# Optimization experiments

Hardware: AMD Instinct MI355X
Metric: run time of the kernel (lower is better)

The kernel has to match this reference:

```python
import jax, jax.numpy as jnp
import numpy as np

N_NODES = 100000
N_EDGES = 3200000
N_FEAT = 256
HIDDEN = 64
N_CLASSES = 6


def gcn_conv(x, W, b, src, dst, n_nodes):
    """PyG GCNConv: out = D^{-1/2} (A + I) D^{-1/2} X W + b (self-loops added)."""
    h = x @ W  # [N, out]
    loops = jnp.arange(n_nodes, dtype=src.dtype)
    src2 = jnp.concatenate([src, loops])
    dst2 = jnp.concatenate([dst, loops])
    # degree over destination nodes (edge weight 1), including self-loops
    deg = jax.ops.segment_sum(jnp.ones_like(dst2, dtype=h.dtype), dst2,
                              num_segments=n_nodes)
    dis = jnp.where(deg > 0, jax.lax.rsqrt(deg), 0.0)  # deg^{-1/2}
    norm = dis[src2] * dis[dst2]  # [E+N]
    msg = h[src2] * norm[:, None]  # gather + scale
    out = jax.ops.segment_sum(msg, dst2, num_segments=n_nodes)  # scatter-add
    return out + b


def setup_inputs() -> dict:
    key = jax.random.key(0)
    ks = jax.random.split(key, 5)
    x = jax.random.normal(ks[0], (N_NODES, N_FEAT), dtype=jnp.float32)
    edge_index = jax.random.randint(ks[1], (2, N_EDGES), 0, N_NODES, dtype=jnp.int64)
    W1 = jax.random.normal(ks[2], (N_FEAT, HIDDEN), dtype=jnp.float32) / np.sqrt(N_FEAT)
    b1 = jnp.zeros((HIDDEN,), dtype=jnp.float32)
    W2 = jax.random.normal(ks[3], (HIDDEN, HIDDEN), dtype=jnp.float32) / np.sqrt(HIDDEN)
    b2 = jnp.zeros((HIDDEN,), dtype=jnp.float32)
    Wfc = jax.random.normal(ks[4], (HIDDEN, N_CLASSES), dtype=jnp.float32) / np.sqrt(HIDDEN)
    bfc = jnp.zeros((N_CLASSES,), dtype=jnp.float32)
    return {"x": x, "edge_index": edge_index, "W1": W1, "b1": b1,
            "W2": W2, "b2": b2, "Wfc": Wfc, "bfc": bfc}


def reference(x, edge_index, W1, b1, W2, b2, Wfc, bfc):
    src, dst = edge_index[0], edge_index[1]
    n = x.shape[0]
    h = jax.nn.relu(gcn_conv(x, W1, b1, src, dst, n))
    # dropout(p=0.2) is identity in eval mode
    h = jax.nn.relu(gcn_conv(h, W2, b2, src, dst, n))
    return h @ Wfc + bfc
```

## Files before the change

kernel.cpp:

```cpp
#include <hip/hip_runtime.h>
#include <hip/hip_fp16.h>
#include <math.h>

#define NFEAT 256
#define HID 64
#define NCLS 6
#define CAP 4096
#define NBMX 1600
#define RCAP 8
#define CHUNK 16384
#define ROUND 1024
#define FUSED_LDS 57856

typedef float vf4 __attribute__((ext_vector_type(4)));
typedef int   vi4 __attribute__((ext_vector_type(4)));


__global__ __launch_bounds__(256) void k_zero_int(int* __restrict__ p, int n) {
  int i = blockIdx.x * 256 + threadIdx.x;
  if (i < n) p[i] = 0;
}


__global__ __launch_bounds__(256) void k_fused(const int* __restrict__ src,
                                               const int* __restrict__ dst,
                                               int* __restrict__ gcur,
                                               unsigned* __restrict__ packed,
                                               int E, int nbuck, int nbb,
                                               const float* __restrict__ X,
                                               const float* __restrict__ W1,
                                               __half* __restrict__ H16, int n) {
  extern __shared__ char smem[];
  int t = threadIdx.x;

  if (blockIdx.x < nbb) {
    unsigned* ring = (unsigned*)smem;
    int* basel = (int*)(smem + NBMX * RCAP * 4);
    for (int i = t; i < nbuck; i += 256) basel[i] = 0;
    __syncthreads();

    int e0 = blockIdx.x * CHUNK;
    int e1 = e0 + CHUNK;
    if (e1 > E) e1 = E;

    for (int r0 = e0; r0 < e1; r0 += ROUND) {
      int i0 = r0 + t * 4;
      int s4[4], d4[4];
      bool full = (i0 + 4 <= e1);
      if (full) {
        vi4 sv = __builtin_nontemporal_load((const vi4*)&src[i0]);
        vi4 dv = __builtin_nontemporal_load((const vi4*)&dst[i0]);
        s4[0] = sv.x; s4[1] = sv.y; s4[2] = sv.z; s4[3] = sv.w;
        d4[0] = dv.x; d4[1] = dv.y; d4[2] = dv.z; d4[3] = dv.w;
      } else {
        for (int q = 0; q < 4; ++q)
          if (i0 + q < e1) { s4[q] = src[i0 + q]; d4[q] = dst[i0 + q]; }
      }
#pragma unroll
      for (int q = 0; q < 4; ++q) {
        if (i0 + q < e1) {
          int b = d4[q] >> 6;
          unsigned e = ((unsigned)s4[q] << 6) | (unsigned)(d4[q] & 63);
          int sl = atomicAdd(&basel[b], 1);
          if (sl < RCAP) ring[b * RCAP + sl] = e;
          else packed[(size_t)b * CAP + atomicAdd(&gcur[b], 1)] = e;
        }
      }
      __syncthreads();
      for (int b = t; b < nbuck; b += 256) {
        if (basel[b] >= RCAP) {
          int gb = atomicAdd(&gcur[b], RCAP);
          unsigned* pd = &packed[(size_t)b * CAP + gb];
#pragma unroll
          for (int k = 0; k < RCAP; ++k) pd[k] = ring[b * RCAP + k];
          basel[b] = 0;
        }
      }
      __syncthreads();
    }
    for (int b = t; b < nbuck; b += 256) {
      int m = basel[b];
      if (m > 0) {
        int gb = atomicAdd(&gcur[b], m);
        unsigned* pd = &packed[(size_t)b * CAP + gb];
        for (int k = 0; k < m; ++k) pd[k] = ring[b * RCAP + k];
      }
    }
  } else {
    float* Wl = (float*)smem;
    float* Xl = Wl + 4096;
    const int row0 = (blockIdx.x - nbb) * 64;
    const int tc = t & 15;
    const int tr = t >> 4;
    float acc[4][4] = {};

    for (int k0 = 0; k0 < NFEAT; k0 += 64) {
      __syncthreads();
#pragma unroll
      for (int i = 0; i < 4; ++i) {
        int idx = t * 4 + i * 1024;
        int kr = idx >> 6, c = idx & 63;
        *(vf4*)&Wl[idx] = *(const vf4*)&W1[(size_t)(k0 + kr) * 64 + c];
      }
#pragma unroll
      for (int i = 0; i < 4; ++i) {
        int idx = t * 4 + i * 1024;
        int r = idx >> 6, c = idx & 63;
        int row = row0 + r;
        vf4 v = {0.f, 0.f, 0.f, 0.f};
        if (row < n) v = __builtin_nontemporal_load((const vf4*)&X[(size_t)row * NFEAT + k0 + c]);
        *(vf4*)&Xl[idx] = v;
      }
      __syncthreads();
#pragma unroll 4
      for (int kk = 0; kk < 64; kk += 4) {
        float4 xv[4], wv[4];
#pragma unroll
        for (int r = 0; r < 4; ++r) xv[r] = *(float4*)&Xl[(tr * 4 + r) * 64 + kk];
#pragma unroll
        for (int q = 0; q < 4; ++q) wv[q] = *(float4*)&Wl[(kk + q) * 64 + tc * 4];
#pragma unroll
        for (int r = 0; r < 4; ++r) {
          const float xr[4] = {xv[r].x, xv[r].y, xv[r].z, xv[r].w};
#pragma unroll
          for (int q = 0; q < 4; ++q) {
            acc[r][0] += xr[q] * wv[q].x;
            acc[r][1] += xr[q] * wv[q].y;
            acc[r][2] += xr[q] * wv[q].z;
            acc[r][3] += xr[q] * wv[q].w;
          }
        }
      }
    }
#pragma unroll
    for (int r = 0; r < 4; ++r) {
      int row = row0 + tr * 4 + r;
      if (row < n) {
        __half2 h01 = __floats2half2_rn(acc[r][0], acc[r][1]);
        __half2 h23 = __floats2half2_rn(acc[r][2], acc[r][3]);
        uint2 st;
        st.x = *reinterpret_cast<unsigned*>(&h01);
        st.y = *reinterpret_cast<unsigned*>(&h23);
        ((uint2*)H16)[(size_t)row * 16 + tc] = st;
      }
    }
  }
}


__global__ __launch_bounds__(256) void k_build(unsigned* __restrict__ packed,
                                               const int* __restrict__ gcur,
                                               int2* __restrict__ rowrange,
                                               float* __restrict__ dis,
                                               int n, int nbuck) {
  __shared__ unsigned buf[CAP];
  __shared__ unsigned outb[CAP];
  __shared__ int cnt4[4][64];
  __shared__ int cur4[4][64];
  __shared__ int offi[64];
  __shared__ int offx[64];
  __shared__ int cntl[64];
  int b = blockIdx.x;
  int t = threadIdx.x;
  int g = t >> 6;
  int m = gcur[b];
  if (m > CAP) m = CAP;
  unsigned* pb = packed + (size_t)b * CAP;

  cnt4[g][t & 63] = 0;
  for (int k = t; k < m; k += 256) buf[k] = pb[k];
  __syncthreads();
  for (int k = t; k < m; k += 256) atomicAdd(&cnt4[g][buf[k] & 63u], 1);
  __syncthreads();
  if (t < 64) {
    int c0 = cnt4[0][t], c1 = cnt4[1][t], c2 = cnt4[2][t], c3 = cnt4[3][t];
    int tot = c0 + c1 + c2 + c3;
    cntl[t] = tot;
    offi[t] = tot;
    cur4[0][t] = 0;
    cur4[1][t] = c0;
    cur4[2][t] = c0 + c1;
    cur4[3][t] = c0 + c1 + c2;
  }
  __syncthreads();
  for (int off = 1; off < 64; off <<= 1) {
    int x = (t < 64) ? offi[t] : 0;
    int y = (t >= off && t < 64) ? offi[t - off] : 0;
    __syncthreads();
    if (t < 64) offi[t] = x + y;
    __syncthreads();
  }
  if (t < 64) {
    offx[t] = offi[t] - cntl[t];
    int v = b * 64 + t;
    if (v < n) {
      rowrange[v] = make_int2(b * CAP + offx[t], cntl[t]);
      dis[v] = rsqrtf((float)cntl[t] + 1.0f);
    }
#pragma unroll
    for (int gg = 0; gg < 4; ++gg) cur4[gg][t] += offx[t];
  }
  __syncthreads();
  for (int k = t; k < m; k += 256) {
    unsigned e = buf[k];
    int dl = e & 63u;
    int q = atomicAdd(&cur4[g][dl], 1);
    outb[q] = e >> 6;
  }
  __syncthreads();
  for (int k = t; k < m; k += 256) pb[k] = outb[k];
}


__global__ __launch_bounds__(256) void k_agg_w(const int2* __restrict__ rowrange,
                                               const int* __restrict__ srcs,
                                               const __half* __restrict__ g16,
                                               const float* __restrict__ dis,
                                               const float* __restrict__ bias,
                                               float* __restrict__ outp, int n) {
  int v = blockIdx.x * 16 + (threadIdx.x >> 4);
  if (v >= n) return;
  int lane = threadIdx.x & 15;
  int2 rr = rowrange[v];
  int j = rr.x, end = rr.x + rr.y;
  const uint2* g2 = (const uint2*)g16;

  float dv = dis[v];
  uint2 su = g2[(size_t)v * 16 + lane];
  float2 f0 = __half22float2(*reinterpret_cast<__half2*>(&su.x));
  float2 f1 = __half22float2(*reinterpret_cast<__half2*>(&su.y));
  float ax = dv * f0.x, ay = dv * f0.y, az = dv * f1.x, aw = dv * f1.y;

  for (; j + 8 <= end; j += 8) {
    int s[8];
#pragma unroll
    for (int q = 0; q < 8; ++q) s[q] = __builtin_nontemporal_load(&srcs[j + q]);
    float ds[8];
    uint2 a[8];
#pragma unroll
    for (int q = 0; q < 8; ++q) { ds[q] = dis[s[q]]; a[q] = g2[(size_t)s[q] * 16 + lane]; }
#pragma unroll
    for (int q = 0; q < 8; ++q) {
      float2 p0 = __half22float2(*reinterpret_cast<__half2*>(&a[q].x));
      float2 p1 = __half22float2(*reinterpret_cast<__half2*>(&a[q].y));
      ax = fmaf(ds[q], p0.x, ax); ay = fmaf(ds[q], p0.y, ay);
      az = fmaf(ds[q], p1.x, az); aw = fmaf(ds[q], p1.y, aw);
    }
  }
  for (; j < end; ++j) {
    int s0 = __builtin_nontemporal_load(&srcs[j]);
    float ds = dis[s0];
    uint2 a0 = g2[(size_t)s0 * 16 + lane];
    float2 p0 = __half22float2(*reinterpret_cast<__half2*>(&a0.x));
    float2 p1 = __half22float2(*reinterpret_cast<__half2*>(&a0.y));
    ax = fmaf(ds, p0.x, ax); ay = fmaf(ds, p0.y, ay);
    az = fmaf(ds, p1.x, az); aw = fmaf(ds, p1.y, aw);
  }

  float4 bb = *(const float4*)&bias[lane * 4];
  float4 o;
  o.x = fmaxf(fmaf(dv, ax, bb.x), 0.f);
  o.y = fmaxf(fmaf(dv, ay, bb.y), 0.f);
  o.z = fmaxf(fmaf(dv, az, bb.z), 0.f);
  o.w = fmaxf(fmaf(dv, aw, bb.w), 0.f);
  ((float4*)outp)[(size_t)v * 16 + lane] = o;
}


template<int K>
__global__ __launch_bounds__(256) void k_gemm_scaled(const float* __restrict__ X,
                                                     const float* __restrict__ W,
                                                     const float* __restrict__ dis,
                                                     __half* __restrict__ G16, int n) {
  __shared__ float Wl[64 * 64];
  __shared__ float Xl[64 * 64];
  const int tid = threadIdx.x;
  const int row0 = blockIdx.x * 64;
  const int tc = tid & 15;
  const int tr = tid >> 4;
  float acc[4][4] = {};

  for (int k0 = 0; k0 < K; k0 += 64) {
    __syncthreads();
#pragma unroll
    for (int i = 0; i < 4; ++i) {
      int idx = tid * 4 + i * 1024;
      int kr = idx >> 6, c = idx & 63;
      *(vf4*)&Wl[idx] = *(const vf4*)&W[(size_t)(k0 + kr) * 64 + c];
    }
#pragma unroll
    for (int i = 0; i < 4; ++i) {
      int idx = tid * 4 + i * 1024;
      int r = idx >> 6, c = idx & 63;
      int row = row0 + r;
      vf4 v = {0.f, 0.f, 0.f, 0.f};
      if (row < n) v = __builtin_nontemporal_load((const vf4*)&X[(size_t)row * K + k0 + c]);
      *(vf4*)&Xl[idx] = v;
    }
    __syncthreads();
#pragma unroll 4
    for (int kk = 0; kk < 64; kk += 4) {
      float4 xv[4], wv[4];
#pragma unroll
      for (int r = 0; r < 4; ++r) xv[r] = *(float4*)&Xl[(tr * 4 + r) * 64 + kk];
#pragma unroll
      for (int q = 0; q < 4; ++q) wv[q] = *(float4*)&Wl[(kk + q) * 64 + tc * 4];
#pragma unroll
      for (int r = 0; r < 4; ++r) {
        const float xr[4] = {xv[r].x, xv[r].y, xv[r].z, xv[r].w};
#pragma unroll
        for (int q = 0; q < 4; ++q) {
          acc[r][0] += xr[q] * wv[q].x;
          acc[r][1] += xr[q] * wv[q].y;
          acc[r][2] += xr[q] * wv[q].z;
          acc[r][3] += xr[q] * wv[q].w;
        }
      }
    }
  }
#pragma unroll
  for (int r = 0; r < 4; ++r) {
    int row = row0 + tr * 4 + r;
    if (row < n) {
      float s = dis[row];
      __half2 h01 = __floats2half2_rn(acc[r][0] * s, acc[r][1] * s);
      __half2 h23 = __floats2half2_rn(acc[r][2] * s, acc[r][3] * s);
      uint2 st;
      st.x = *reinterpret_cast<unsigned*>(&h01);
      st.y = *reinterpret_cast<unsigned*>(&h23);
      ((uint2*)G16)[(size_t)row * 16 + tc] = st;
    }
  }
}


__global__ __launch_bounds__(256) void k_agg_csr(const int2* __restrict__ rowrange,
                                                 const int* __restrict__ srcs,
                                                 const __half* __restrict__ g16,
                                                 const float* __restrict__ dis,
                                                 const float* __restrict__ bias,
                                                 float* __restrict__ outp, int n) {
  int v = blockIdx.x * 16 + (threadIdx.x >> 4);
  if (v >= n) return;
  int lane = threadIdx.x & 15;
  int2 rr = rowrange[v];
  int j = rr.x, end = rr.x + rr.y;
  const uint2* g2 = (const uint2*)g16;

  uint2 su = g2[(size_t)v * 16 + lane];
  float2 f0 = __half22float2(*reinterpret_cast<__half2*>(&su.x));
  float2 f1 = __half22float2(*reinterpret_cast<__half2*>(&su.y));
  float ax = f0.x, ay = f0.y, az = f1.x, aw = f1.y;

  for (; j + 8 <= end; j += 8) {
    int s[8];
#pragma unroll
    for (int q = 0; q < 8; ++q) s[q] = __builtin_nontemporal_load(&srcs[j + q]);
    uint2 a[8];
#pragma unroll
    for (int q = 0; q < 8; ++q) a[q] = g2[(size_t)s[q] * 16 + lane];
#pragma unroll
    for (int q = 0; q < 8; ++q) {
      float2 p0 = __half22float2(*reinterpret_cast<__half2*>(&a[q].x));
      float2 p1 = __half22float2(*reinterpret_cast<__half2*>(&a[q].y));
      ax += p0.x; ay += p0.y; az += p1.x; aw += p1.y;
    }
  }
  for (; j < end; ++j) {
    int s0 = __builtin_nontemporal_load(&srcs[j]);
    uint2 a0 = g2[(size_t)s0 * 16 + lane];
    float2 p0 = __half22float2(*reinterpret_cast<__half2*>(&a0.x));
    float2 p1 = __half22float2(*reinterpret_cast<__half2*>(&a0.y));
    ax += p0.x; ay += p0.y; az += p1.x; aw += p1.y;
  }

  float dv = dis[v];
  float4 bb = *(const float4*)&bias[lane * 4];
  float4 o;
  o.x = fmaxf(fmaf(dv, ax, bb.x), 0.f);
  o.y = fmaxf(fmaf(dv, ay, bb.y), 0.f);
  o.z = fmaxf(fmaf(dv, az, bb.z), 0.f);
  o.w = fmaxf(fmaf(dv, aw, bb.w), 0.f);
  ((float4*)outp)[(size_t)v * 16 + lane] = o;
}


__global__ __launch_bounds__(256) void k_fc(const float* __restrict__ A,
                                            const float* __restrict__ Wfc,
                                            const float* __restrict__ bfc,
                                            float* __restrict__ outp, int n) {
  __shared__ float Wl[64 * NCLS];
  __shared__ float bl[8];
  int tid = threadIdx.x;
  for (int i = tid; i < 64 * NCLS; i += 256) Wl[i] = Wfc[i];
  if (tid < NCLS) bl[tid] = bfc[tid];
  __syncthreads();
  int row = blockIdx.x * 256 + tid;
  if (row >= n) return;
  float accv[NCLS];
#pragma unroll
  for (int j = 0; j < NCLS; ++j) accv[j] = bl[j];
  const vf4* a4 = (const vf4*)&A[(size_t)row * 64];
#pragma unroll
  for (int k4 = 0; k4 < 16; ++k4) {
    vf4 a = __builtin_nontemporal_load(&a4[k4]);
    const float av[4] = {a.x, a.y, a.z, a.w};
#pragma unroll
    for (int q = 0; q < 4; ++q)
#pragma unroll
      for (int j = 0; j < NCLS; ++j) accv[j] += av[q] * Wl[(k4 * 4 + q) * NCLS + j];
  }
#pragma unroll
  for (int j = 0; j < NCLS; ++j) outp[(size_t)row * NCLS + j] = accv[j];
}


extern "C" void kernel_launch(void* const* d_in, const int* in_sizes, int n_in,
                              void* d_out, int out_size, void* d_ws, size_t ws_size,
                              hipStream_t stream) {
  const float* x   = (const float*)d_in[0];
  const int*   ei  = (const int*)d_in[1];
  const float* W1  = (const float*)d_in[2];
  const float* b1  = (const float*)d_in[3];
  const float* W2  = (const float*)d_in[4];
  const float* b2  = (const float*)d_in[5];
  const float* Wfc = (const float*)d_in[6];
  const float* bfc = (const float*)d_in[7];
  float* out = (float*)d_out;

  const int n = in_sizes[0] / NFEAT;
  const int E = in_sizes[1] / 2;
  const int* src = ei;
  const int* dst = ei + E;
  const int nbuck = (n + 63) >> 6;
  const int nbb = (E + CHUNK - 1) / CHUNK;
  const int ntile = (n + 63) / 64;

  char* ws = (char*)d_ws;
  size_t off = 0;
  auto alloc = [&](size_t bytes) -> void* {
    void* p = (void*)(ws + off);
    off += (bytes + 255) & ~(size_t)255;
    return p;
  };
  float* dis      = (float*)alloc((size_t)n * 4);
  int2*  rowrange = (int2*)alloc((size_t)n * 8);
  int*   gcur     = (int*)alloc((size_t)nbuck * 4);
  unsigned* packed = (unsigned*)alloc((size_t)nbuck * CAP * 4);
  __half* bufA16  = (__half*)alloc((size_t)n * HID * 2);
  float* bufB     = (float*)alloc((size_t)n * HID * 4);

  k_zero_int<<<(nbuck + 255) / 256, 256, 0, stream>>>(gcur, nbuck);
  k_fused<<<nbb + ntile, 256, FUSED_LDS, stream>>>(src, dst, gcur, packed, E, nbuck, nbb,
                                                   x, W1, bufA16, n);
  k_build<<<nbuck, 256, 0, stream>>>(packed, gcur, rowrange, dis, n, nbuck);

  k_agg_w<<<(n + 15) / 16, 256, 0, stream>>>(rowrange, (const int*)packed, bufA16, dis, b1, bufB, n);

  k_gemm_scaled<HID><<<(n + 63) / 64, 256, 0, stream>>>(bufB, W2, dis, bufA16, n);
  k_agg_csr<<<(n + 15) / 16, 256, 0, stream>>>(rowrange, (const int*)packed, bufA16, dis, b2, bufB, n);

  k_fc<<<(n + 255) / 256, 256, 0, stream>>>(bufB, Wfc, bfc, out, n);
}
```

Before: 319.8 us.

## Replace atomic bucket rings with count-scan-scatter edge bucketing

Replaces the LDS ring-buffer plus global-atomic bucketing of edges with a two-pass scheme. A count kernel builds per-block bucket histograms, a single-block scan turns them into exact offsets, and the fused kernel then scatters edges directly to precomputed slots in a compact E-sized array. This removes the global atomics and per-round syncs, and drops the fixed per-bucket capacity padding. The cost is an extra read of dst, two added launches, and a serial single-block scan over about 196x1563 counts.

```diff
diff --git a/kernel.cpp b/kernel.cpp
--- a/kernel.cpp
+++ b/kernel.cpp
@@ -5,26 +5,95 @@
 #define NFEAT 256
 #define HID 64
 #define NCLS 6
-#define CAP 4096
 #define NBMX 1600
-#define RCAP 8
+#define CAPB 4096
 #define CHUNK 16384
-#define ROUND 1024
-#define FUSED_LDS 57856
+#define FUSED_LDS 32768
 
 typedef float vf4 __attribute__((ext_vector_type(4)));
 typedef int   vi4 __attribute__((ext_vector_type(4)));
 
 
-__global__ __launch_bounds__(256) void k_zero_int(int* __restrict__ p, int n) {
-  int i = blockIdx.x * 256 + threadIdx.x;
-  if (i < n) p[i] = 0;
+__global__ __launch_bounds__(256) void k_count(const int* __restrict__ dst,
+                                               int* __restrict__ C, int E, int nbuck) {
+  __shared__ int cnt[NBMX];
+  int t = threadIdx.x;
+  for (int i = t; i < nbuck; i += 256) cnt[i] = 0;
+  __syncthreads();
+  int e0 = blockIdx.x * CHUNK;
+  int e1 = e0 + CHUNK;
+  if (e1 > E) e1 = E;
+  for (int r0 = e0; r0 < e1; r0 += 1024) {
+    int i0 = r0 + t * 4;
+    if (i0 + 4 <= e1) {
+      vi4 dv = __builtin_nontemporal_load((const vi4*)&dst[i0]);
+      atomicAdd(&cnt[dv.x >> 6], 1);
+      atomicAdd(&cnt[dv.y >> 6], 1);
+      atomicAdd(&cnt[dv.z >> 6], 1);
+      atomicAdd(&cnt[dv.w >> 6], 1);
+    } else {
+      for (int q = 0; q < 4; ++q)
+        if (i0 + q < e1) atomicAdd(&cnt[dst[i0 + q] >> 6], 1);
+    }
+  }
+  __syncthreads();
+  int* Crow = C + (size_t)blockIdx.x * nbuck;
+  for (int i = t; i < nbuck; i += 256) Crow[i] = cnt[i];
+}
+
+
+__global__ __launch_bounds__(256) void k_scan(int* __restrict__ C,
+                                              int* __restrict__ T,
+                                              int* __restrict__ bbase,
+                                              int nblk, int nbuck) {
+  __shared__ int sh[256];
+  __shared__ int carry;
+  int t = threadIdx.x;
+  for (int b = t; b < nbuck; b += 256) {
+    int run = 0;
+    int blk = 0;
+    for (; blk + 4 <= nblk; blk += 4) {
+      int c0 = C[(size_t)(blk + 0) * nbuck + b];
+      int c1 = C[(size_t)(blk + 1) * nbuck + b];
+      int c2 = C[(size_t)(blk + 2) * nbuck + b];
+      int c3 = C[(size_t)(blk + 3) * nbuck + b];
+      C[(size_t)(blk + 0) * nbuck + b] = run; run += c0;
+      C[(size_t)(blk + 1) * nbuck + b] = run; run += c1;
+      C[(size_t)(blk + 2) * nbuck + b] = run; run += c2;
+      C[(size_t)(blk + 3) * nbuck + b] = run; run += c3;
+    }
+    for (; blk < nblk; ++blk) {
+      int c = C[(size_t)blk * nbuck + b];
+      C[(size_t)blk * nbuck + b] = run;
+      run += c;
+    }
+    T[b] = run;
+  }
+  if (t == 0) carry = 0;
+  __syncthreads();
+  for (int base = 0; base < nbuck; base += 256) {
+    int v = (base + t < nbuck) ? T[base + t] : 0;
+    sh[t] = v;
+    __syncthreads();
+    for (int off = 1; off < 256; off <<= 1) {
+      int x = sh[t];
+      int y = (t >= off) ? sh[t - off] : 0;
+      __syncthreads();
+      sh[t] = x + y;
+      __syncthreads();
+    }
+    if (base + t < nbuck) bbase[base + t] = carry + sh[t] - v;
+    __syncthreads();
+    if (t == 255) carry += sh[255];
+    __syncthreads();
+  }
 }
 
 
 __global__ __launch_bounds__(256) void k_fused(const int* __restrict__ src,
                                                const int* __restrict__ dst,
-                                               int* __restrict__ gcur,
+                                               const int* __restrict__ C,
+                                               const int* __restrict__ bbase,
                                                unsigned* __restrict__ packed,
                                                int E, int nbuck, int nbb,
                                                const float* __restrict__ X,
@@ -34,16 +103,19 @@
   int t = threadIdx.x;
 
   if (blockIdx.x < nbb) {
-    unsigned* ring = (unsigned*)smem;
-    int* basel = (int*)(smem + NBMX * RCAP * 4);
-    for (int i = t; i < nbuck; i += 256) basel[i] = 0;
+    int* baseL = (int*)smem;
+    int* cnt   = baseL + NBMX;
+    const int* Crow = C + (size_t)blockIdx.x * nbuck;
+    for (int i = t; i < nbuck; i += 256) {
+      baseL[i] = bbase[i] + Crow[i];
+      cnt[i] = 0;
+    }
     __syncthreads();
 
     int e0 = blockIdx.x * CHUNK;
     int e1 = e0 + CHUNK;
     if (e1 > E) e1 = E;
-
-    for (int r0 = e0; r0 < e1; r0 += ROUND) {
+    for (int r0 = e0; r0 < e1; r0 += 1024) {
       int i0 = r0 + t * 4;
       int s4[4], d4[4];
       bool full = (i0 + 4 <= e1);
@@ -60,30 +132,10 @@
       for (int q = 0; q < 4; ++q) {
         if (i0 + q < e1) {
           int b = d4[q] >> 6;
-          unsigned e = ((unsigned)s4[q] << 6) | (unsigned)(d4[q] & 63);
-          int sl = atomicAdd(&basel[b], 1);
-          if (sl < RCAP) ring[b * RCAP + sl] = e;
-          else packed[(size_t)b * CAP + atomicAdd(&gcur[b], 1)] = e;
+          int slot = atomicAdd(&cnt[b], 1);
+          packed[(size_t)baseL[b] + slot] =
+              ((unsigned)s4[q] << 6) | (unsigned)(d4[q] & 63);
         }
-      }
-      __syncthreads();
-      for (int b = t; b < nbuck; b += 256) {
-        if (basel[b] >= RCAP) {
-          int gb = atomicAdd(&gcur[b], RCAP);
-          unsigned* pd = &packed[(size_t)b * CAP + gb];
-#pragma unroll
-          for (int k = 0; k < RCAP; ++k) pd[k] = ring[b * RCAP + k];
-          basel[b] = 0;
-        }
-      }
-      __syncthreads();
-    }
-    for (int b = t; b < nbuck; b += 256) {
-      int m = basel[b];
-      if (m > 0) {
-        int gb = atomicAdd(&gcur[b], m);
-        unsigned* pd = &packed[(size_t)b * CAP + gb];
-        for (int k = 0; k < m; ++k) pd[k] = ring[b * RCAP + k];
       }
     }
   } else {
@@ -149,12 +201,13 @@
 
 
 __global__ __launch_bounds__(256) void k_build(unsigned* __restrict__ packed,
-                                               const int* __restrict__ gcur,
+                                               const int* __restrict__ T,
+                                               const int* __restrict__ bbase,
                                                int2* __restrict__ rowrange,
                                                float* __restrict__ dis,
                                                int n, int nbuck) {
-  __shared__ unsigned buf[CAP];
-  __shared__ unsigned outb[CAP];
+  __shared__ unsigned buf[CAPB];
+  __shared__ unsigned outb[CAPB];
   __shared__ int cnt4[4][64];
   __shared__ int cur4[4][64];
   __shared__ int offi[64];
@@ -163,9 +216,10 @@
   int b = blockIdx.x;
   int t = threadIdx.x;
   int g = t >> 6;
-  int m = gcur[b];
-  if (m > CAP) m = CAP;
-  unsigned* pb = packed + (size_t)b * CAP;
+  int m = T[b];
+  if (m > CAPB) m = CAPB;
+  int bb = bbase[b];
+  unsigned* pb = packed + bb;
 
   cnt4[g][t & 63] = 0;
   for (int k = t; k < m; k += 256) buf[k] = pb[k];
@@ -194,7 +248,7 @@
     offx[t] = offi[t] - cntl[t];
     int v = b * 64 + t;
     if (v < n) {
-      rowrange[v] = make_int2(b * CAP + offx[t], cntl[t]);
+      rowrange[v] = make_int2(bb + offx[t], cntl[t]);
       dis[v] = rsqrtf((float)cntl[t] + 1.0f);
     }
 #pragma unroll
@@ -445,15 +499,18 @@
   };
   float* dis      = (float*)alloc((size_t)n * 4);
   int2*  rowrange = (int2*)alloc((size_t)n * 8);
-  int*   gcur     = (int*)alloc((size_t)nbuck * 4);
-  unsigned* packed = (unsigned*)alloc((size_t)nbuck * CAP * 4);
+  int*   C        = (int*)alloc((size_t)nbb * nbuck * 4);
+  int*   T        = (int*)alloc((size_t)nbuck * 4);
+  int*   bbase    = (int*)alloc((size_t)nbuck * 4);
+  unsigned* packed = (unsigned*)alloc((size_t)E * 4);
   __half* bufA16  = (__half*)alloc((size_t)n * HID * 2);
   float* bufB     = (float*)alloc((size_t)n * HID * 4);
 
-  k_zero_int<<<(nbuck + 255) / 256, 256, 0, stream>>>(gcur, nbuck);
-  k_fused<<<nbb + ntile, 256, FUSED_LDS, stream>>>(src, dst, gcur, packed, E, nbuck, nbb,
-                                                   x, W1, bufA16, n);
-  k_build<<<nbuck, 256, 0, stream>>>(packed, gcur, rowrange, dis, n, nbuck);
+  k_count<<<nbb, 256, 0, stream>>>(dst, C, E, nbuck);
+  k_scan<<<1, 256, 0, stream>>>(C, T, bbase, nbb, nbuck);
+  k_fused<<<nbb + ntile, 256, FUSED_LDS, stream>>>(src, dst, C, bbase, packed,
+                                                   E, nbuck, nbb, x, W1, bufA16, n);
+  k_build<<<nbuck, 256, 0, stream>>>(packed, T, bbase, rowrange, dis, n, nbuck);
 
   k_agg_w<<<(n + 15) / 16, 256, 0, stream>>>(rowrange, (const int*)packed, bufA16, dis, b1, bufB, n);
 
```

After: 399.0 us. 1.25x slower.
